# Performance work log

Hardware: AMD Instinct MI355X
Metric: run time of the kernel (lower is better)

The kernel has to match this reference:

```python
import jax, jax.numpy as jnp
import numpy as np

C = 256
G = 32  # GroupNorm groups
EPS = 1e-6


def setup_inputs() -> dict:
    key = jax.random.key(0)
    ks = jax.random.split(key, 11)
    B, H, W = 4, 64, 64
    scale = 0.02
    return {
        "x": jax.random.normal(ks[0], (B, C, H, W), dtype=jnp.float32),
        "gn_scale": jnp.ones((C,), jnp.float32),
        "gn_bias": jnp.zeros((C,), jnp.float32),
        "wq": jax.random.normal(ks[1], (C, C), jnp.float32) * scale,
        "bq": jnp.zeros((C,), jnp.float32),
        "wk": jax.random.normal(ks[2], (C, C), jnp.float32) * scale,
        "bk": jnp.zeros((C,), jnp.float32),
        "wv": jax.random.normal(ks[3], (C, C), jnp.float32) * scale,
        "bv": jnp.zeros((C,), jnp.float32),
        "wp": jax.random.normal(ks[4], (C, C), jnp.float32) * scale,
        "bp": jnp.zeros((C,), jnp.float32),
    }


def _group_norm(x, scale, bias):
    b, c, h, w = x.shape
    xr = x.reshape(b, G, c // G, h, w)
    mu = jnp.mean(xr, axis=(2, 3, 4), keepdims=True)
    var = jnp.var(xr, axis=(2, 3, 4), keepdims=True)
    xn = ((xr - mu) * jax.lax.rsqrt(var + EPS)).reshape(b, c, h, w)
    return xn * scale[None, :, None, None] + bias[None, :, None, None]


def _conv1x1(x, w, bch):
    # 1x1 conv == channel-mixing matmul; w is (out_ch, in_ch)
    return jnp.einsum('bchw,dc->bdhw', x, w) + bch[None, :, None, None]


def reference(x, gn_scale, gn_bias, wq, bq, wk, bk, wv, bv, wp, bp):
    b, c, h, w = x.shape
    hn = _group_norm(x, gn_scale, gn_bias)
    q = _conv1x1(hn, wq, bq).reshape(b, c, h * w)  # (b,c,N)
    k = _conv1x1(hn, wk, bk).reshape(b, c, h * w)
    v = _conv1x1(hn, wv, bv).reshape(b, c, h * w)
    # attn[b,i,j] = softmax_j( q_i . k_j / sqrt(c) )
    attn = jax.nn.softmax(jnp.einsum('bci,bcj->bij', q, k) * (c ** -0.5), axis=-1)
    A = jnp.einsum('bcj,bij->bci', v, attn).reshape(b, c, h, w)
    return x + _conv1x1(A, wp, bp)
```

## Files before the change

kernel.cpp:

```cpp
#include <hip/hip_runtime.h>
#include <stdint.h>

#define Bn 4
#define Cn 256
#define Gn 32
#define Nn 4096
#define CGn 8

typedef unsigned short u16;
typedef __attribute__((ext_vector_type(8))) short short8;
typedef __attribute__((ext_vector_type(4))) short short4v;
typedef __attribute__((ext_vector_type(4))) float f32x4;
typedef __attribute__((ext_vector_type(16))) float f32x16;

__device__ __forceinline__ u16 f2bf(float x) {
  uint32_t u = __float_as_uint(x);
  u += 0x7fffu + ((u >> 16) & 1u);
  return (u16)(u >> 16);
}
__device__ __forceinline__ float b2f(u16 v) {
  return __uint_as_float(((uint32_t)v) << 16);
}

__device__ __forceinline__ void gl_lds16(const void* g, void* l) {
  __builtin_amdgcn_global_load_lds(
      (__attribute__((address_space(1))) void*)(uintptr_t)g,
      (__attribute__((address_space(3))) void*)(uintptr_t)l, 16, 0, 0);
}

__device__ __forceinline__ int sw512(int row, int cb) { return row * 512 + ((cb ^ (row & 7)) * 16); }

__global__ void k_cs(const float* __restrict__ wq, const float* __restrict__ wk,
                     const float* __restrict__ wv, const float* __restrict__ wp,
                     const float* __restrict__ bq, const float* __restrict__ bk,
                     const float* __restrict__ bv, const float* __restrict__ x,
                     u16* __restrict__ wqkv, u16* __restrict__ wpb,
                     float* __restrict__ bqkv, float* __restrict__ stats) {
  if (blockIdx.x < 256) {
    const float s = 0.09016844005556021f;
    int i = blockIdx.x * 256 + threadIdx.x;
    wqkv[i]          = f2bf(wq[i] * s);
    wqkv[i + 65536]  = f2bf(wk[i]);
    wqkv[i + 131072] = f2bf(wv[i]);
    wpb[i]           = f2bf(wp[i]);
    if (i < 256) { bqkv[i] = bq[i] * s; bqkv[i + 256] = bk[i]; bqkv[i + 512] = bv[i]; }
  } else {
    int blk = blockIdx.x - 256;
    int grp = blk >> 2, part = blk & 3;
    const float4* base = (const float4*)(x + (size_t)grp * (CGn * Nn) + part * 8192);
    float s = 0.f, s2 = 0.f;
    for (int i = threadIdx.x; i < 2048; i += 256) {
      float4 v = base[i];
      s  += v.x + v.y + v.z + v.w;
      s2 += v.x * v.x + v.y * v.y + v.z * v.z + v.w * v.w;
    }
#pragma unroll
    for (int m = 1; m < 64; m <<= 1) { s += __shfl_xor(s, m, 64); s2 += __shfl_xor(s2, m, 64); }
    __shared__ float ps[4], ps2[4];
    int w = threadIdx.x >> 6;
    if ((threadIdx.x & 63) == 0) { ps[w] = s; ps2[w] = s2; }
    __syncthreads();
    if (threadIdx.x == 0) {
      stats[grp * 8 + part * 2]     = ps[0] + ps[1] + ps[2] + ps[3];
      stats[grp * 8 + part * 2 + 1] = ps2[0] + ps2[1] + ps2[2] + ps2[3];
    }
  }
}

__global__ void k_apply(const float* __restrict__ x, const float* __restrict__ stats,
                        const float* __restrict__ gsc, const float* __restrict__ gbi,
                        u16* __restrict__ hnT) {
  __shared__ __align__(16) char smem[32768];
  __shared__ float smu[Gn], srs[Gn];
  int n0 = blockIdx.x * 64;
  int b = blockIdx.y;
  int tid = threadIdx.x;
  if (tid < Gn) {
    float S = 0.f, S2 = 0.f;
#pragma unroll
    for (int p = 0; p < 4; ++p) {
      S  += stats[(b * Gn + tid) * 8 + p * 2];
      S2 += stats[(b * Gn + tid) * 8 + p * 2 + 1];
    }
    const float inv = 1.f / (CGn * Nn);
    float mu = S * inv;
    float var = S2 * inv - mu * mu;
    smu[tid] = mu;
    srs[tid] = rsqrtf(var + 1e-6f);
  }
  __syncthreads();
  int nl = (tid & 15) * 4;
  int cbase = tid >> 4;
  for (int pass = 0; pass < 16; ++pass) {
    int c = pass * 16 + cbase;
    float4 v = *(const float4*)(x + (size_t)b * Cn * Nn + (size_t)c * Nn + n0 + nl);
    int g = c >> 3;
    float sc = gsc[c] * srs[g];
    float bi = gbi[c] - smu[g] * sc;
    float vals[4] = {v.x, v.y, v.z, v.w};
#pragma unroll
    for (int i = 0; i < 4; ++i) {
      int row = nl + i;
      int off = row * 512 + ((((c >> 3) + row) & 31) * 16) + (c & 7) * 2;
      *(u16*)(smem + off) = f2bf(vals[i] * sc + bi);
    }
  }
  __syncthreads();
#pragma unroll
  for (int p = 0; p < 8; ++p) {
    int idx = p * 256 + tid;
    int row = idx >> 5, pc = idx & 31;
    int gc = (pc - row) & 31;
    short8 v8 = *(const short8*)(smem + row * 512 + pc * 16);
    *(short8*)(hnT + ((size_t)b * Nn + n0 + row) * Cn + gc * 8) = v8;
  }
}

__global__ __launch_bounds__(256, 2)
void k_qkv(const u16* __restrict__ wqkv, const float* __restrict__ bqkv,
           const u16* __restrict__ hnT, u16* __restrict__ qT, u16* __restrict__ kT,
           u16* __restrict__ vv) {
  __shared__ __align__(16) char smem[65536];
  int tid = threadIdx.x, lane = tid & 63, w = tid >> 6, quad = lane >> 4, low = lane & 15;
  int n0 = blockIdx.x * 64, d0 = blockIdx.y * 64, b = blockIdx.z;
  {
    int r0 = w * 16;
#pragma unroll
    for (int s = 0; s < 8; ++s) {
      int rs = r0 + s * 2;
      int r = rs + (lane >> 5);
      int cb = (lane & 31) ^ (r & 7);
      gl_lds16(wqkv + (size_t)(d0 + r) * Cn + cb * 8, smem + rs * 512);
      gl_lds16(hnT + ((size_t)b * Nn + n0 + r) * Cn + cb * 8, smem + 32768 + rs * 512);
    }
  }
  asm volatile("s_waitcnt vmcnt(0)" ::: "memory");
  __syncthreads();
  f32x4 acc[4] = {{0.f,0.f,0.f,0.f},{0.f,0.f,0.f,0.f},{0.f,0.f,0.f,0.f},{0.f,0.f,0.f,0.f}};
#pragma unroll
  for (int kk = 0; kk < 8; ++kk) {
    short8 af = *(const short8*)(smem + sw512(w * 16 + low, kk * 4 + quad));
#pragma unroll
    for (int t = 0; t < 4; ++t) {
      short8 bf = *(const short8*)(smem + 32768 + sw512(t * 16 + low, kk * 4 + quad));
      acc[t] = __builtin_amdgcn_mfma_f32_16x16x32_bf16(af, bf, acc[t], 0, 0, 0);
    }
  }
  int which = d0 >> 8;
  float bias[4];
#pragma unroll
  for (int r = 0; r < 4; ++r) bias[r] = bqkv[d0 + w * 16 + quad * 4 + r];
  __syncthreads();
  if (which == 2) {
#pragma unroll
    for (int t = 0; t < 4; ++t)
#pragma unroll
      for (int r = 0; r < 4; ++r) {
        int row = w * 16 + quad * 4 + r;
        int col = t * 16 + low;
        int off = row * 128 + ((((col >> 3) ^ ((row >> 1) & 7)) & 7) * 16) + (col & 7) * 2;
        *(u16*)(smem + off) = f2bf(acc[t][r] + bias[r]);
      }
  } else {
#pragma unroll
    for (int t = 0; t < 4; ++t)
#pragma unroll
      for (int r = 0; r < 4; ++r) {
        int row = t * 16 + low;
        int col = w * 16 + quad * 4 + r;
        int off = row * 128 + ((((col >> 3) ^ ((row >> 1) & 7)) & 7) * 16) + (col & 7) * 2;
        *(u16*)(smem + off) = f2bf(acc[t][r] + bias[r]);
      }
  }
  __syncthreads();
  int dl0 = d0 & 255;
#pragma unroll
  for (int p = 0; p < 2; ++p) {
    int idx = p * 256 + tid;
    int row = idx >> 3, pc = idx & 7;
    int cb = pc ^ ((row >> 1) & 7);
    short8 v8 = *(const short8*)(smem + row * 128 + pc * 16);
    if (which == 2)
      *(short8*)(vv + (size_t)b * Cn * Nn + (size_t)(dl0 + row) * Nn + n0 + cb * 8) = v8;
    else {
      u16* dst = (which == 0 ? qT : kT) + (size_t)b * Nn * Cn;
      *(short8*)(dst + (size_t)(n0 + row) * Cn + dl0 + cb * 8) = v8;
    }
  }
}

__device__ __forceinline__ void flash_stage(char* smem, int bsel, const u16* kTb,
                                            const u16* vb, int j0, int w, int lo,
                                            int kr, int vr, int vp) {
  char* ksb = smem + bsel * 32768;
  char* vsb = ksb + 16384;
#pragma unroll
  for (int s = 0; s < 4; ++s) {
    int j = kr + s * 2;
    int gc = (lo - j) & 31;
    gl_lds16(kTb + (size_t)(j0 + j) * Cn + gc * 8, ksb + (w * 8 + s * 2) * 512);
  }
#pragma unroll
  for (int s = 0; s < 4; ++s) {
    int c = vr + s * 16;
    int gc = (vp - c - (c >> 2)) & 3;
    gl_lds16(vb + (size_t)c * Nn + j0 + gc * 8, vsb + (w * 64 + s * 16) * 64);
  }
}

__global__ __launch_bounds__(256, 2)
void k_flash(const u16* __restrict__ qT, const u16* __restrict__ kT,
             const u16* __restrict__ vv, u16* __restrict__ Op0,
             u16* __restrict__ Op1, u16* __restrict__ Op2, u16* __restrict__ Op3,
             float* __restrict__ lrow) {
  __shared__ __align__(16) char smem[65536];
  const int tid = threadIdx.x, lane = tid & 63, w = tid >> 6;
  const int lo = lane & 31, hi = lane >> 5;
  const int i0 = blockIdx.x * 128;
  const int b = blockIdx.y, jh = blockIdx.z;
  const u16* qTb = qT + (size_t)b * Nn * Cn;
  const u16* kTb = kT + (size_t)b * Nn * Cn;
  const u16* vb  = vv + (size_t)b * Cn * Nn;
  const int u7 = lo + hi;
  const int u9 = lo + hi + (lo >> 2);
  const int kr = w * 8 + hi;
  const int vr = w * 64 + (lane >> 2);
  const int vp = lane & 3;

  flash_stage(smem, 0, kTb, vb, jh * 1024, w, lo, kr, vr, vp);

  short8 qf[16];
  {
    const u16* qrow = qTb + (size_t)(i0 + w * 32 + lo) * Cn + hi * 8;
#pragma unroll
    for (int ks = 0; ks < 16; ++ks) qf[ks] = *(const short8*)(qrow + ks * 16);
  }
  f32x16 Oa[8];
#pragma unroll
  for (int ct = 0; ct < 8; ++ct)
#pragma unroll
    for (int e = 0; e < 16; ++e) Oa[ct][e] = 0.f;
  float l_ = 0.f;

  for (int jt = 0; jt < 32; ++jt) {
    if (jt < 31) {
      flash_stage(smem, (jt + 1) & 1, kTb, vb, jh * 1024 + (jt + 1) * 32, w, lo, kr, vr, vp);
      asm volatile("s_waitcnt vmcnt(8)" ::: "memory");
    } else {
      asm volatile("s_waitcnt vmcnt(0)" ::: "memory");
    }
    asm volatile("s_barrier" ::: "memory");
    const char* ksb = smem + (jt & 1) * 32768;
    const char* vsb = ksb + 16384;

    f32x16 S0;
#pragma unroll
    for (int e = 0; e < 16; ++e) S0[e] = 0.f;
#pragma unroll
    for (int ks = 0; ks < 16; ++ks) {
      int ch = (ks * 2 + u7) & 31;
      short8 a0 = *(const short8*)(ksb + lo * 512 + ch * 16);
      S0 = __builtin_amdgcn_mfma_f32_32x32x16_bf16(a0, qf[ks], S0, 0, 0, 0);
    }
    uint32_t Pp[8];
#pragma unroll
    for (int g = 0; g < 8; ++g) {
      float p0 = __builtin_amdgcn_exp2f(S0[2 * g]);
      float p1 = __builtin_amdgcn_exp2f(S0[2 * g + 1]);
      l_ += p0 + p1;
      Pp[g] = ((uint32_t)f2bf(p1) << 16) | f2bf(p0);
    }
#pragma unroll
    for (int kst = 0; kst < 2; ++kst) {
      uint32_t a0 = Pp[4 * kst], a1 = Pp[4 * kst + 1];
      uint32_t b0 = Pp[4 * kst + 2], b1 = Pp[4 * kst + 3];
      uint32_t s0 = hi ? a0 : b0, s1 = hi ? a1 : b1;
      uint32_t r0 = (uint32_t)__shfl_xor((int)s0, 32, 64);
      uint32_t r1 = (uint32_t)__shfl_xor((int)s1, 32, 64);
      union { uint32_t u[4]; short8 s8; } pu;
      pu.u[0] = hi ? r0 : a0;
      pu.u[1] = hi ? r1 : a1;
      pu.u[2] = hi ? b0 : r0;
      pu.u[3] = hi ? b1 : r1;
      int ch = (kst * 2 + u9) & 3;
#pragma unroll
      for (int ct = 0; ct < 8; ++ct) {
        short8 vf = *(const short8*)(vsb + (ct * 32 + lo) * 64 + ch * 16);
        Oa[ct] = __builtin_amdgcn_mfma_f32_32x32x16_bf16(vf, pu.s8, Oa[ct], 0, 0, 0);
      }
    }
    asm volatile("s_barrier" ::: "memory");
  }

  l_ += __shfl_xor(l_, 32, 64);
  if (hi == 0)
    lrow[(size_t)jh * (Bn * Nn) + (size_t)b * Nn + i0 + w * 32 + lo] = l_;
  float invl = __builtin_amdgcn_rcpf(l_);
  __syncthreads();
#pragma unroll
  for (int ct = 0; ct < 8; ++ct)
#pragma unroll
    for (int g = 0; g < 4; ++g) {
      short4v pk;
#pragma unroll
      for (int r = 0; r < 4; ++r) pk[r] = (short)f2bf(Oa[ct][g * 4 + r] * invl);
      int chv = (ct * 4 + g + lo) & 31;
      *(short4v*)(smem + w * 16384 + lo * 512 + chv * 16 + hi * 8) = pk;
    }
  __syncthreads();
  u16* Opj = (jh == 0) ? Op0 : (jh == 1) ? Op1 : (jh == 2) ? Op2 : Op3;
  u16* Ob = Opj + ((size_t)b * Nn + i0 + w * 32) * (size_t)Cn;
#pragma unroll
  for (int s = 0; s < 16; ++s) {
    int rr = s * 2 + hi;
    short8 v8 = *(const short8*)(smem + w * 16384 + rr * 512 + lo * 16);
    int gc = (lo - rr) & 31;
    *(short8*)(Ob + (size_t)rr * Cn + gc * 8) = v8;
  }
}

__global__ void k_comb(const u16* __restrict__ O0, const u16* __restrict__ O1,
                       const u16* __restrict__ O2, const u16* __restrict__ O3,
                       const float* __restrict__ lrow, u16* __restrict__ OT) {
  int gid = blockIdx.x * 256 + threadIdx.x;
  int row = gid >> 6;
  int c4 = (gid & 63) << 2;
  float L = lrow[row] + lrow[Bn * Nn + row] + lrow[2 * Bn * Nn + row] + lrow[3 * Bn * Nn + row];
  float inv = __builtin_amdgcn_rcpf(L);
  size_t base = (size_t)row * Cn + c4;
  short4v a0 = *(const short4v*)(O0 + base);
  short4v a1 = *(const short4v*)(O1 + base);
  short4v a2 = *(const short4v*)(O2 + base);
  short4v a3 = *(const short4v*)(O3 + base);
  short4v o;
#pragma unroll
  for (int i = 0; i < 4; ++i)
    o[i] = (short)f2bf((b2f((u16)a0[i]) + b2f((u16)a1[i]) + b2f((u16)a2[i]) + b2f((u16)a3[i])) * inv);
  *(short4v*)(OT + base) = o;
}

__global__ __launch_bounds__(256, 2)
void k_proj(const u16* __restrict__ wpb, const float* __restrict__ bp,
            const u16* __restrict__ OT, const float* __restrict__ x,
            float* __restrict__ out) {
  __shared__ __align__(16) char smem[65536];
  int tid = threadIdx.x, lane = tid & 63, w = tid >> 6, quad = lane >> 4, low = lane & 15;
  int n0 = blockIdx.x * 64, d0 = blockIdx.y * 64, b = blockIdx.z;
  {
    int r0 = w * 16;
#pragma unroll
    for (int s = 0; s < 8; ++s) {
      int rs = r0 + s * 2;
      int r = rs + (lane >> 5);
      int cb = (lane & 31) ^ (r & 7);
      gl_lds16(wpb + (size_t)(d0 + r) * Cn + cb * 8, smem + rs * 512);
      gl_lds16(OT + ((size_t)b * Nn + n0 + r) * Cn + cb * 8, smem + 32768 + rs * 512);
    }
  }
  asm volatile("s_waitcnt vmcnt(0)" ::: "memory");
  __syncthreads();
  f32x4 acc[4] = {{0.f,0.f,0.f,0.f},{0.f,0.f,0.f,0.f},{0.f,0.f,0.f,0.f},{0.f,0.f,0.f,0.f}};
#pragma unroll
  for (int kk = 0; kk < 8; ++kk) {
    short8 af = *(const short8*)(smem + sw512(w * 16 + low, kk * 4 + quad));
#pragma unroll
    for (int t = 0; t < 4; ++t) {
      short8 bf = *(const short8*)(smem + 32768 + sw512(t * 16 + low, kk * 4 + quad));
      acc[t] = __builtin_amdgcn_mfma_f32_16x16x32_bf16(af, bf, acc[t], 0, 0, 0);
    }
  }
  int dloc = d0 + w * 16 + quad * 4;
#pragma unroll
  for (int t = 0; t < 4; ++t)
#pragma unroll
    for (int r = 0; r < 4; ++r) {
      size_t idx = (size_t)b * Cn * Nn + (size_t)(dloc + r) * Nn + n0 + t * 16 + low;
      out[idx] = x[idx] + acc[t][r] + bp[dloc + r];
    }
}

extern "C" void kernel_launch(void* const* d_in, const int* in_sizes, int n_in,
                              void* d_out, int out_size, void* d_ws, size_t ws_size,
                              hipStream_t stream) {
  const float* x   = (const float*)d_in[0];
  const float* gsc = (const float*)d_in[1];
  const float* gbi = (const float*)d_in[2];
  const float* wq  = (const float*)d_in[3];
  const float* bq  = (const float*)d_in[4];
  const float* wk  = (const float*)d_in[5];
  const float* bk  = (const float*)d_in[6];
  const float* wv  = (const float*)d_in[7];
  const float* bv  = (const float*)d_in[8];
  const float* wp  = (const float*)d_in[9];
  const float* bp  = (const float*)d_in[10];
  float* out = (float*)d_out;

  char* ws = (char*)d_ws;
  u16*   wqkv  = (u16*)(ws + 0);
  u16*   wpb   = (u16*)(ws + 393216);
  float* bqkv  = (float*)(ws + 524288);
  float* stats = (float*)(ws + 527360);
  float* lrow  = (float*)(ws + 532480);
  u16*   hnT   = (u16*)(ws + 1048576);
  u16*   qT    = (u16*)(ws + 9437184);
  u16*   kT    = (u16*)(ws + 17825792);
  u16*   vv    = (u16*)(ws + 26214400);
  u16*   Op1   = (u16*)(ws + 34603008);
  u16*   Op2   = (u16*)(ws + 42991616);
  u16*   Op3   = (u16*)(ws + 51380224);

  k_cs<<<768, 256, 0, stream>>>(wq, wk, wv, wp, bq, bk, bv, x, wqkv, wpb, bqkv, stats);
  k_apply<<<dim3(64, 4), 256, 0, stream>>>(x, stats, gsc, gbi, hnT);
  k_qkv<<<dim3(64, 12, 4), 256, 0, stream>>>(wqkv, bqkv, hnT, qT, kT, vv);
  k_flash<<<dim3(32, 4, 4), 256, 0, stream>>>(qT, kT, vv, hnT , Op1, Op2, Op3, lrow);
  k_comb<<<4096, 256, 0, stream>>>(hnT, Op1, Op2, Op3, lrow, qT );
  k_proj<<<dim3(64, 4, 4), 256, 0, stream>>>(wpb, bp, qT , x, out);
}
```

Baseline: 202.5 us.

## Software-pipeline PV matmul one tile behind QK and split QK accumulator chain

Restructures the flash-attention inner loop so the P·V MFMAs for tile jt-1 run at the start of iteration jt, before the next K/V tile is staged. This overlaps them with the global loads and with the QK^T of the current tile, and a tail block handles the last tile. The QK^T reduction is split into two independent accumulators to shorten the MFMA dependency chain. The bf16 conversion of P switches from round-to-nearest to truncation via a byte permute, which costs slightly less precision.

```diff
diff --git a/kernel.cpp b/kernel.cpp
--- a/kernel.cpp
+++ b/kernel.cpp
@@ -241,8 +241,32 @@
 #pragma unroll
     for (int e = 0; e < 16; ++e) Oa[ct][e] = 0.f;
   float l_ = 0.f;
+  uint32_t Pp[8];
 
   for (int jt = 0; jt < 32; ++jt) {
+    if (jt > 0) {
+      const char* vsb = smem + ((jt + 1) & 1) * 32768 + 16384;
+#pragma unroll
+      for (int kst = 0; kst < 2; ++kst) {
+        uint32_t a0 = Pp[4 * kst], a1 = Pp[4 * kst + 1];
+        uint32_t b0 = Pp[4 * kst + 2], b1 = Pp[4 * kst + 3];
+        uint32_t s0 = hi ? a0 : b0, s1 = hi ? a1 : b1;
+        uint32_t r0 = (uint32_t)__shfl_xor((int)s0, 32, 64);
+        uint32_t r1 = (uint32_t)__shfl_xor((int)s1, 32, 64);
+        union { uint32_t u[4]; short8 s8; } pu;
+        pu.u[0] = hi ? r0 : a0;
+        pu.u[1] = hi ? r1 : a1;
+        pu.u[2] = hi ? b0 : r0;
+        pu.u[3] = hi ? b1 : r1;
+        int ch = (kst * 2 + u9) & 3;
+#pragma unroll
+        for (int ct = 0; ct < 8; ++ct) {
+          short8 vf = *(const short8*)(vsb + (ct * 32 + lo) * 64 + ch * 16);
+          Oa[ct] = __builtin_amdgcn_mfma_f32_32x32x16_bf16(vf, pu.s8, Oa[ct], 0, 0, 0);
+        }
+      }
+    }
+    asm volatile("s_barrier" ::: "memory");
     if (jt < 31) {
       flash_stage(smem, (jt + 1) & 1, kTb, vb, jh * 1024 + (jt + 1) * 32, w, lo, kr, vr, vp);
       asm volatile("s_waitcnt vmcnt(8)" ::: "memory");
@@ -251,25 +275,29 @@
     }
     asm volatile("s_barrier" ::: "memory");
     const char* ksb = smem + (jt & 1) * 32768;
-    const char* vsb = ksb + 16384;
-
-    f32x16 S0;
-#pragma unroll
-    for (int e = 0; e < 16; ++e) S0[e] = 0.f;
-#pragma unroll
-    for (int ks = 0; ks < 16; ++ks) {
-      int ch = (ks * 2 + u7) & 31;
-      short8 a0 = *(const short8*)(ksb + lo * 512 + ch * 16);
-      S0 = __builtin_amdgcn_mfma_f32_32x32x16_bf16(a0, qf[ks], S0, 0, 0, 0);
-    }
-    uint32_t Pp[8];
+
+    f32x16 Sa, Sb;
+#pragma unroll
+    for (int e = 0; e < 16; ++e) { Sa[e] = 0.f; Sb[e] = 0.f; }
+#pragma unroll
+    for (int ks = 0; ks < 16; ks += 2) {
+      int ch0 = (ks * 2 + u7) & 31;
+      int ch1 = (ks * 2 + 2 + u7) & 31;
+      short8 a0 = *(const short8*)(ksb + lo * 512 + ch0 * 16);
+      short8 a1 = *(const short8*)(ksb + lo * 512 + ch1 * 16);
+      Sa = __builtin_amdgcn_mfma_f32_32x32x16_bf16(a0, qf[ks], Sa, 0, 0, 0);
+      Sb = __builtin_amdgcn_mfma_f32_32x32x16_bf16(a1, qf[ks + 1], Sb, 0, 0, 0);
+    }
 #pragma unroll
     for (int g = 0; g < 8; ++g) {
-      float p0 = __builtin_amdgcn_exp2f(S0[2 * g]);
-      float p1 = __builtin_amdgcn_exp2f(S0[2 * g + 1]);
+      float p0 = __builtin_amdgcn_exp2f(Sa[2 * g] + Sb[2 * g]);
+      float p1 = __builtin_amdgcn_exp2f(Sa[2 * g + 1] + Sb[2 * g + 1]);
       l_ += p0 + p1;
-      Pp[g] = ((uint32_t)f2bf(p1) << 16) | f2bf(p0);
-    }
+      Pp[g] = __builtin_amdgcn_perm(__float_as_uint(p1), __float_as_uint(p0), 0x07060302u);
+    }
+  }
+  {
+    const char* vsb = smem + 32768 + 16384;
 #pragma unroll
     for (int kst = 0; kst < 2; ++kst) {
       uint32_t a0 = Pp[4 * kst], a1 = Pp[4 * kst + 1];
@@ -289,7 +317,6 @@
         Oa[ct] = __builtin_amdgcn_mfma_f32_32x32x16_bf16(vf, pu.s8, Oa[ct], 0, 0, 0);
       }
     }
-    asm volatile("s_barrier" ::: "memory");
   }
 
   l_ += __shfl_xor(l_, 32, 64);
```

Measured after the change: 227.0 us. 1.12x slower.

## Pipeline QKV projection over four N-tiles with register-resident weights

Applied to the files above, without the earlier changes.

Each k_qkv block now handles four 64-column N tiles instead of one, so the grid shrinks by 4x. The weight fragments are loaded once into registers instead of being staged through LDS, and the hnT tiles are double-buffered with async global-to-LDS loads so the next tile loads while the current one is multiplied. The epilogue uses a per-wave LDS transpose region with padded strides instead of a block-wide swizzled one. The cost is fewer blocks in flight and higher register pressure from holding the weight fragments.

```diff
diff --git a/kernel.cpp b/kernel.cpp
--- a/kernel.cpp
+++ b/kernel.cpp
@@ -121,72 +121,89 @@
            const u16* __restrict__ hnT, u16* __restrict__ qT, u16* __restrict__ kT,
            u16* __restrict__ vv) {
   __shared__ __align__(16) char smem[65536];
-  int tid = threadIdx.x, lane = tid & 63, w = tid >> 6, quad = lane >> 4, low = lane & 15;
-  int n0 = blockIdx.x * 64, d0 = blockIdx.y * 64, b = blockIdx.z;
+  const int tid = threadIdx.x, lane = tid & 63, w = tid >> 6;
+  const int quad = (lane >> 4) & 3, low = lane & 15;
+  const int d0 = blockIdx.y * 64, b = blockIdx.z;
+  const int n_base = blockIdx.x * 256;
+  const int which = d0 >> 8;
+  const int dl0 = d0 & 255;
+  const u16* hb = hnT + (size_t)b * Nn * Cn;
+  const int scol = lane & 31;
+
+#define QKV_STAGE(bsel, nt)                                                     \
+  {                                                                             \
+    _Pragma("unroll") for (int s = 0; s < 8; ++s) {                             \
+      int r = w * 16 + s * 2 + (lane >> 5);                                     \
+      int gc = (scol - r) & 31;                                                 \
+      gl_lds16(hb + (size_t)(n_base + (nt) * 64 + r) * Cn + gc * 8,             \
+               smem + (bsel) * 32768 + (w * 16 + s * 2) * 512);                 \
+    }                                                                           \
+  }
+
+  QKV_STAGE(0, 0);
+  short8 af[8];
   {
-    int r0 = w * 16;
-#pragma unroll
-    for (int s = 0; s < 8; ++s) {
-      int rs = r0 + s * 2;
-      int r = rs + (lane >> 5);
-      int cb = (lane & 31) ^ (r & 7);
-      gl_lds16(wqkv + (size_t)(d0 + r) * Cn + cb * 8, smem + rs * 512);
-      gl_lds16(hnT + ((size_t)b * Nn + n0 + r) * Cn + cb * 8, smem + 32768 + rs * 512);
-    }
-  }
-  asm volatile("s_waitcnt vmcnt(0)" ::: "memory");
-  __syncthreads();
-  f32x4 acc[4] = {{0.f,0.f,0.f,0.f},{0.f,0.f,0.f,0.f},{0.f,0.f,0.f,0.f},{0.f,0.f,0.f,0.f}};
-#pragma unroll
-  for (int kk = 0; kk < 8; ++kk) {
-    short8 af = *(const short8*)(smem + sw512(w * 16 + low, kk * 4 + quad));
-#pragma unroll
-    for (int t = 0; t < 4; ++t) {
-      short8 bf = *(const short8*)(smem + 32768 + sw512(t * 16 + low, kk * 4 + quad));
-      acc[t] = __builtin_amdgcn_mfma_f32_16x16x32_bf16(af, bf, acc[t], 0, 0, 0);
-    }
-  }
-  int which = d0 >> 8;
+    const u16* wrow = wqkv + (size_t)(d0 + w * 16 + low) * Cn + quad * 8;
+#pragma unroll
+    for (int kk = 0; kk < 8; ++kk) af[kk] = *(const short8*)(wrow + kk * 32);
+  }
   float bias[4];
 #pragma unroll
   for (int r = 0; r < 4; ++r) bias[r] = bqkv[d0 + w * 16 + quad * 4 + r];
-  __syncthreads();
-  if (which == 2) {
-#pragma unroll
-    for (int t = 0; t < 4; ++t)
-#pragma unroll
-      for (int r = 0; r < 4; ++r) {
-        int row = w * 16 + quad * 4 + r;
-        int col = t * 16 + low;
-        int off = row * 128 + ((((col >> 3) ^ ((row >> 1) & 7)) & 7) * 16) + (col & 7) * 2;
-        *(u16*)(smem + off) = f2bf(acc[t][r] + bias[r]);
+
+  for (int nt = 0; nt < 4; ++nt) {
+    if (nt < 3) {
+      QKV_STAGE((nt + 1) & 1, nt + 1);
+      asm volatile("s_waitcnt vmcnt(10)" ::: "memory");
+    } else {
+      asm volatile("s_waitcnt vmcnt(0)" ::: "memory");
+    }
+    asm volatile("s_barrier" ::: "memory");
+    char* buf = smem + (nt & 1) * 32768;
+    f32x4 acc[4] = {{0.f,0.f,0.f,0.f},{0.f,0.f,0.f,0.f},{0.f,0.f,0.f,0.f},{0.f,0.f,0.f,0.f}};
+#pragma unroll
+    for (int kk = 0; kk < 8; ++kk)
+#pragma unroll
+      for (int t = 0; t < 4; ++t) {
+        int row = t * 16 + low;
+        short8 bf = *(const short8*)(buf + row * 512 + (((kk * 4 + quad) + row) & 31) * 16);
+        acc[t] = __builtin_amdgcn_mfma_f32_16x16x32_bf16(af[kk], bf, acc[t], 0, 0, 0);
       }
-  } else {
-#pragma unroll
-    for (int t = 0; t < 4; ++t)
-#pragma unroll
-      for (int r = 0; r < 4; ++r) {
-        int row = t * 16 + low;
-        int col = w * 16 + quad * 4 + r;
-        int off = row * 128 + ((((col >> 3) ^ ((row >> 1) & 7)) & 7) * 16) + (col & 7) * 2;
-        *(u16*)(smem + off) = f2bf(acc[t][r] + bias[r]);
+    asm volatile("s_barrier" ::: "memory");
+    char* Q = buf + w * 8192;
+    if (which == 2) {
+#pragma unroll
+      for (int t = 0; t < 4; ++t)
+#pragma unroll
+        for (int r = 0; r < 4; ++r)
+          *(u16*)(Q + (quad * 4 + r) * 144 + t * 32 + low * 2) = f2bf(acc[t][r] + bias[r]);
+#pragma unroll
+      for (int s = 0; s < 2; ++s) {
+        int slot = s * 64 + lane;
+        int row = slot >> 3, ch = slot & 7;
+        short8 v8 = *(const short8*)(Q + row * 144 + ch * 16);
+        *(short8*)(vv + (size_t)b * Cn * Nn + (size_t)(dl0 + w * 16 + row) * Nn +
+                   n_base + nt * 64 + ch * 8) = v8;
       }
-  }
-  __syncthreads();
-  int dl0 = d0 & 255;
-#pragma unroll
-  for (int p = 0; p < 2; ++p) {
-    int idx = p * 256 + tid;
-    int row = idx >> 3, pc = idx & 7;
-    int cb = pc ^ ((row >> 1) & 7);
-    short8 v8 = *(const short8*)(smem + row * 128 + pc * 16);
-    if (which == 2)
-      *(short8*)(vv + (size_t)b * Cn * Nn + (size_t)(dl0 + row) * Nn + n0 + cb * 8) = v8;
-    else {
+    } else {
+#pragma unroll
+      for (int t = 0; t < 4; ++t) {
+        short4v pk;
+#pragma unroll
+        for (int r = 0; r < 4; ++r) pk[r] = (short)f2bf(acc[t][r] + bias[r]);
+        *(short4v*)(Q + (t * 16 + low) * 48 + quad * 8) = pk;
+      }
       u16* dst = (which == 0 ? qT : kT) + (size_t)b * Nn * Cn;
-      *(short8*)(dst + (size_t)(n0 + row) * Cn + dl0 + cb * 8) = v8;
-    }
-  }
+#pragma unroll
+      for (int s = 0; s < 2; ++s) {
+        int slot = s * 64 + lane;
+        int row = slot >> 1, half = slot & 1;
+        short8 v8 = *(const short8*)(Q + row * 48 + half * 16);
+        *(short8*)(dst + (size_t)(n_base + nt * 64 + row) * Cn + dl0 + w * 16 + half * 8) = v8;
+      }
+    }
+  }
+#undef QKV_STAGE
 }
 
 __device__ __forceinline__ void flash_stage(char* smem, int bsel, const u16* kTb,
@@ -411,7 +428,7 @@
 
   k_cs<<<768, 256, 0, stream>>>(wq, wk, wv, wp, bq, bk, bv, x, wqkv, wpb, bqkv, stats);
   k_apply<<<dim3(64, 4), 256, 0, stream>>>(x, stats, gsc, gbi, hnT);
-  k_qkv<<<dim3(64, 12, 4), 256, 0, stream>>>(wqkv, bqkv, hnT, qT, kT, vv);
+  k_qkv<<<dim3(16, 12, 4), 256, 0, stream>>>(wqkv, bqkv, hnT, qT, kT, vv);
   k_flash<<<dim3(32, 4, 4), 256, 0, stream>>>(qT, kT, vv, hnT , Op1, Op2, Op3, lrow);
   k_comb<<<4096, 256, 0, stream>>>(hnT, Op1, Op2, Op3, lrow, qT );
   k_proj<<<dim3(64, 4, 4), 256, 0, stream>>>(wpb, bp, qT , x, out);
```

Result: no change. 201.0 us (-0.7%).
